# Optimization experiments

Measured on AMD Instinct MI355X. Metric: run time of the kernel, lower is better.

The kernel has to match this reference:

```python
import jax, jax.numpy as jnp
import numpy as np

B, S, C, H = 8, 1024, 768, 8
D = C // H  # head dim = 96
MLP = 4 * C


def setup_inputs() -> dict:
    key = jax.random.key(0)
    ks = jax.random.split(key, 12)
    sc = 0.02
    return {
        "x": jax.random.normal(ks[0], (B, S, C), jnp.float32),
        "ln1_w": jnp.ones((S, C), jnp.float32),
        "ln1_b": jnp.zeros((S, C), jnp.float32),
        "ln2_w": jnp.ones((S, C), jnp.float32),
        "ln2_b": jnp.zeros((S, C), jnp.float32),
        "qkv_w": jax.random.normal(ks[1], (C, 3 * C), jnp.float32) * sc,
        "proj_w": jax.random.normal(ks[2], (C, C), jnp.float32) * sc,
        "mlp_w1": jax.random.normal(ks[3], (C, MLP), jnp.float32) * sc,
        "mlp_b1": jnp.zeros((MLP,), jnp.float32),
        "mlp_w2": jax.random.normal(ks[4], (MLP, C), jnp.float32) * sc,
        "mlp_b2": jnp.zeros((C,), jnp.float32),
    }


def _layernorm2d(x, w, b, eps=1e-5):
    # normalizes over BOTH (seq, channel) dims, per nn.LayerNorm([length, channel])
    mu = jnp.mean(x, axis=(-2, -1), keepdims=True)
    var = jnp.mean(jnp.square(x - mu), axis=(-2, -1), keepdims=True)
    return (x - mu) * jax.lax.rsqrt(var + eps) * w + b


def _attention(x, qkv_w, proj_w):
    b, s, _ = x.shape
    qkv = (x @ qkv_w).reshape(b, s, 3, H, D)
    q, k, v = qkv[:, :, 0], qkv[:, :, 1], qkv[:, :, 2]  # [b, s, h, d]
    # NOTE: original module applies NO 1/sqrt(d) scaling
    scores = jnp.einsum("bshd,bthd->bhst", q, k)
    attn = jax.nn.softmax(scores, axis=-1)
    out = jnp.einsum("bhst,bthd->bshd", attn, v).reshape(b, s, C)
    return out @ proj_w


def reference(x, ln1_w, ln1_b, ln2_w, ln2_b, qkv_w, proj_w, mlp_w1, mlp_b1, mlp_w2, mlp_b2):
    # dropout is identity in eval mode
    h = x + _attention(_layernorm2d(x, ln1_w, ln1_b), qkv_w, proj_w)
    y = _layernorm2d(h, ln2_w, ln2_b)
    y = jax.nn.gelu(y @ mlp_w1 + mlp_b1, approximate=False)
    return h + (y @ mlp_w2 + mlp_b2)
```

## Files before the change

### kernel.cpp

```cpp
#include <hip/hip_runtime.h>
#include <hip/hip_bf16.h>

#define S_LEN 1024
#define NB 8
#define NC 768
#define NH 8
#define HD 96
#define NMLP 3072
#define SC (S_LEN*NC)
#define BS (NB*S_LEN)

typedef __attribute__((ext_vector_type(8))) unsigned short u16x8;
typedef __attribute__((ext_vector_type(4))) unsigned short u16x4;
typedef __attribute__((ext_vector_type(8))) __bf16 bf16x8;
typedef __attribute__((ext_vector_type(4))) float f32x4;

__device__ __forceinline__ unsigned short f2b(float f) {
  union { __hip_bfloat16 h; unsigned short u; } cvt;
  cvt.h = __float2bfloat16(f);
  return cvt.u;
}

__device__ __forceinline__ void gload16(const unsigned short* g, unsigned short* l) {
  __builtin_amdgcn_global_load_lds(
      (const __attribute__((address_space(1))) unsigned int*)g,
      (__attribute__((address_space(3))) unsigned int*)l, 16, 0, 0);
}

__device__ __forceinline__ float gelu_f(float v) {
  float u = v * (0.7978845608f + 0.0356774081f * v * v);
  float au = fabsf(u);
  float e = __expf(-2.0f * au);
  float th = (1.0f - e) / (1.0f + e);
  th = copysignf(th, u);
  return 0.5f * v * (1.0f + th);
}

template<int EPI>
__global__ __launch_bounds__(512, 1)
void gemmks(const unsigned short* __restrict__ A, int lda,
            const unsigned short* __restrict__ Bt, int ldb,
            void* __restrict__ Cv, int ldc, int K,
            const float* __restrict__ bias,
            const float* __restrict__ residual, int ldr,
            float* __restrict__ lnred)
{
  __shared__ unsigned short As[4*4096];
  __shared__ unsigned short Bs[4*8192];
  const int tid = threadIdx.x, lane = tid & 63, wid = tid >> 6;
  const int r15 = lane & 15, g = lane >> 4;
  const int tm = blockIdx.x * 128, tn = blockIdx.y * 256;
  const int NT = K >> 6;

  const int sa = lane >> 3, sc = lane & 7, slc = sc ^ sa;
  const int skc = (slc & 3) << 3;
  const int arow = wid*16 + sa*2 + ((slc >> 2) & 1);
  const unsigned short* Ag  = A  + (size_t)(tm + arow)*lda + skc;
  const unsigned short* Bg0 = Bt + (size_t)(tn + arow)*ldb + skc;
  const unsigned short* Bg1 = Bt + (size_t)(tn + 128 + arow)*ldb + skc;

  const int prl = r15 >> 1;
  const int rdo = prl*128 + (((((r15 & 1) << 2) | g) ^ prl) << 4);
  char* AsB = (char*)As; char* BsB = (char*)Bs;

#define STG(h,kk,b) { \
    gload16(Ag  + (kk) + (h)*32, As + ((b)*2+(h))*4096 + wid*512); \
    gload16(Bg0 + (kk) + (h)*32, Bs + ((b)*2+(h))*8192 + wid*512); \
    gload16(Bg1 + (kk) + (h)*32, Bs + ((b)*2+(h))*8192 + 4096 + wid*512); }
#define MFMA(a8,b8,c) __builtin_amdgcn_mfma_f32_16x16x32_bf16(a8,b8,c,0,0,0)

  f32x4 acc[8][2];
  #pragma unroll
  for (int m = 0; m < 8; ++m) {
    acc[m][0] = (f32x4){0.f,0.f,0.f,0.f};
    acc[m][1] = (f32x4){0.f,0.f,0.f,0.f};
  }

  STG(0,0,0); STG(1,0,0);

  for (int t = 0; t < NT; ++t) {
    const int rd = t & 1, wr = rd ^ 1;
    const int kk = (t + 1) << 6;
    const bool pre = (t + 1) < NT;
    #pragma unroll
    for (int h = 0; h < 2; ++h) {
      if (pre || h == 0) asm volatile("s_waitcnt vmcnt(3)" ::: "memory");
      else               asm volatile("s_waitcnt vmcnt(0)" ::: "memory");
      __builtin_amdgcn_s_barrier();
      const int ab = (rd*2 + h)*8192;
      const int bb = (rd*2 + h)*16384;
      bf16x8 a[8], b[2];
      #pragma unroll
      for (int m = 0; m < 8; ++m) a[m] = *(const bf16x8*)(AsB + ab + m*1024 + rdo);
      b[0] = *(const bf16x8*)(BsB + bb + wid*2048 + rdo);
      b[1] = *(const bf16x8*)(BsB + bb + wid*2048 + 1024 + rdo);
      if (pre) STG(h, kk, wr);
      asm volatile("s_waitcnt lgkmcnt(0)" ::: "memory");
      __builtin_amdgcn_s_setprio(1);
      #pragma unroll
      for (int m = 0; m < 8; ++m) {
        acc[m][0] = MFMA(a[m], b[0], acc[m][0]);
        acc[m][1] = MFMA(a[m], b[1], acc[m][1]);
      }
      __builtin_amdgcn_s_setprio(0);
    }
  }
#undef STG
#undef MFMA

  unsigned short* Cu = (unsigned short*)Cv;
  float* Cf = (float*)Cv;
  float s1 = 0.f, s2 = 0.f;
  #pragma unroll
  for (int m = 0; m < 8; ++m) {
    #pragma unroll
    for (int n = 0; n < 2; ++n) {
      const int col = tn + wid*32 + n*16 + r15;
      #pragma unroll
      for (int r = 0; r < 4; ++r) {
        const int row = tm + m*16 + g*4 + r;
        float v = acc[m][n][r];
        if (EPI == 2 || EPI == 4) v += bias[col];
        if (EPI == 3 || EPI == 4) v += residual[(size_t)row*ldr + col];
        if (EPI == 2) v = gelu_f(v);
        if (EPI == 3) { s1 += v; s2 += v*v; }
        if (EPI == 0 || EPI == 2) Cu[(size_t)row*ldc + col] = f2b(v);
        else                      Cf[(size_t)row*ldc + col] = v;
      }
    }
  }
  if (EPI == 3) {
    #pragma unroll
    for (int o = 32; o; o >>= 1) { s1 += __shfl_xor(s1, o); s2 += __shfl_xor(s2, o); }
    __syncthreads();
    float* red = (float*)As;
    if (lane == 0) { red[wid*2] = s1; red[wid*2+1] = s2; }
    __syncthreads();
    if (tid == 0) {
      float a1 = 0.f, a2 = 0.f;
      #pragma unroll
      for (int w = 0; w < 8; ++w) { a1 += red[w*2]; a2 += red[w*2+1]; }
      const int bidx = tm >> 10;
      atomicAdd(&lnred[bidx*2],     a1);
      atomicAdd(&lnred[bidx*2 + 1], a2);
    }
  }
}

__global__ __launch_bounds__(256, 2)
void flash_attn(const unsigned short* __restrict__ qkv,
                const unsigned short* __restrict__ vt,
                unsigned short* __restrict__ outb)
{
  __shared__ unsigned short Ks[128*96];
  __shared__ unsigned short Vs[96*128];
  __shared__ unsigned short Ps[128*128];
  const int tid = threadIdx.x, lane = tid & 63, wq = tid >> 6;
  const int r15 = lane & 15, g = lane >> 4;
  const int bh = blockIdx.y, b = bh >> 3, h = bh & 7;
  const int q0 = blockIdx.x * 128;
  const int swz = (r15 & 7) << 4;
  char* PsB = (char*)Ps;
  char* VsB = (char*)Vs;

  bf16x8 qf[2][3];
  {
    const unsigned short* qb = qkv + ((size_t)b*S_LEN + q0 + wq*32 + r15)*2304 + h*HD + g*8;
    #pragma unroll
    for (int n = 0; n < 2; ++n)
      #pragma unroll
      for (int kc = 0; kc < 3; ++kc)
        qf[n][kc] = *(const bf16x8*)(qb + (size_t)n*16*2304 + kc*32);
  }

  int krow[6], kcol[6], vrow[6], vcol[6];
  #pragma unroll
  for (int i = 0; i < 6; ++i) {
    const int c = (wq*6 + i)*64 + lane;
    krow[i] = c / 12;
    kcol[i] = (c % 12) * 8;
    const int L = c * 16;
    const int row = L >> 8, cb = L & 255;
    vrow[i] = row;
    vcol[i] = (cb ^ ((row & 7) << 4)) >> 1;
  }
  const unsigned short* kbase = qkv + (size_t)b*S_LEN*2304 + NC + h*HD;
  const unsigned short* vbase = vt + (size_t)bh*HD*S_LEN;

  f32x4 oacc[6][2];
  #pragma unroll
  for (int m = 0; m < 6; ++m) {
    oacc[m][0] = (f32x4){0.f,0.f,0.f,0.f};
    oacc[m][1] = (f32x4){0.f,0.f,0.f,0.f};
  }
  float mrun[2] = {-INFINITY, -INFINITY};
  float lrun[2] = {0.f, 0.f};

  for (int kt = 0; kt < 8; ++kt) {
    const unsigned short* ksrc = kbase + (size_t)kt*128*2304;
    const unsigned short* vsrc = vbase + kt*128;
    #pragma unroll
    for (int i = 0; i < 6; ++i) {
      gload16(ksrc + (size_t)krow[i]*2304 + kcol[i], Ks + (wq*6 + i)*512);
      gload16(vsrc + vrow[i]*1024 + vcol[i],         Vs + (wq*6 + i)*512);
    }
    __syncthreads();

    f32x4 sacc[8][2];
    #pragma unroll
    for (int m = 0; m < 8; ++m) {
      sacc[m][0] = (f32x4){0.f,0.f,0.f,0.f};
      sacc[m][1] = (f32x4){0.f,0.f,0.f,0.f};
    }
    __builtin_amdgcn_s_setprio(1);
    #pragma unroll
    for (int kc = 0; kc < 3; ++kc)
      #pragma unroll
      for (int m = 0; m < 8; ++m) {
        bf16x8 kf = *(const bf16x8*)(Ks + (m*16 + r15)*96 + kc*32 + g*8);
        sacc[m][0] = __builtin_amdgcn_mfma_f32_16x16x32_bf16(kf, qf[0][kc], sacc[m][0], 0,0,0);
        sacc[m][1] = __builtin_amdgcn_mfma_f32_16x16x32_bf16(kf, qf[1][kc], sacc[m][1], 0,0,0);
      }
    __builtin_amdgcn_s_setprio(0);

    #pragma unroll
    for (int n = 0; n < 2; ++n) {
      float pm = -INFINITY;
      #pragma unroll
      for (int m = 0; m < 8; ++m)
        #pragma unroll
        for (int r = 0; r < 4; ++r) pm = fmaxf(pm, sacc[m][n][r]);
      pm = fmaxf(pm, __shfl_xor(pm, 16));
      pm = fmaxf(pm, __shfl_xor(pm, 32));
      const float newm = fmaxf(mrun[n], pm);
      const float scale = __expf(mrun[n] - newm);
      mrun[n] = newm;
      const int qloc = wq*32 + n*16 + r15;
      float s = 0.f;
      #pragma unroll
      for (int m = 0; m < 8; ++m) {
        float e0 = __expf(sacc[m][n][0] - newm);
        float e1 = __expf(sacc[m][n][1] - newm);
        float e2 = __expf(sacc[m][n][2] - newm);
        float e3 = __expf(sacc[m][n][3] - newm);
        s += (e0 + e1) + (e2 + e3);
        u16x4 pk = { f2b(e0), f2b(e1), f2b(e2), f2b(e3) };
        *(u16x4*)(PsB + ((qloc*256 + m*32 + g*8) ^ swz)) = pk;
      }
      s += __shfl_xor(s, 16);
      s += __shfl_xor(s, 32);
      lrun[n] = lrun[n]*scale + s;
      #pragma unroll
      for (int m = 0; m < 6; ++m) oacc[m][n] *= scale;
    }

    #pragma unroll
    for (int kc = 0; kc < 4; ++kc) {
      bf16x8 pf0 = *(const bf16x8*)(PsB + (((wq*32      + r15)*256 + kc*64 + g*16) ^ swz));
      bf16x8 pf1 = *(const bf16x8*)(PsB + (((wq*32 + 16 + r15)*256 + kc*64 + g*16) ^ swz));
      __builtin_amdgcn_s_setprio(1);
      #pragma unroll
      for (int m = 0; m < 6; ++m) {
        bf16x8 vf = *(const bf16x8*)(VsB + (((m*16 + r15)*256 + kc*64 + g*16) ^ swz));
        oacc[m][0] = __builtin_amdgcn_mfma_f32_16x16x32_bf16(vf, pf0, oacc[m][0], 0,0,0);
        oacc[m][1] = __builtin_amdgcn_mfma_f32_16x16x32_bf16(vf, pf1, oacc[m][1], 0,0,0);
      }
      __builtin_amdgcn_s_setprio(0);
    }
    __syncthreads();
  }

  #pragma unroll
  for (int n = 0; n < 2; ++n) {
    const float inv = 1.0f / lrun[n];
    unsigned short* orow = outb + ((size_t)b*S_LEN + q0 + wq*32 + n*16 + r15)*NC + h*HD;
    #pragma unroll
    for (int m = 0; m < 6; ++m) {
      u16x4 pk = { f2b(oacc[m][n][0]*inv), f2b(oacc[m][n][1]*inv),
                   f2b(oacc[m][n][2]*inv), f2b(oacc[m][n][3]*inv) };
      *(u16x4*)(orow + m*16 + g*4) = pk;
    }
  }
}

__global__ void transpose_cast(const float* __restrict__ W, unsigned short* __restrict__ Wt,
                               int K, int N)
{
  __shared__ float tile[32][33];
  const int tx = threadIdx.x & 31, ty = threadIdx.x >> 5;
  const int n0 = blockIdx.x * 32, k0 = blockIdx.y * 32;
  #pragma unroll
  for (int i = 0; i < 32; i += 8)
    tile[ty + i][tx] = W[(size_t)(k0 + ty + i)*N + n0 + tx];
  __syncthreads();
  #pragma unroll
  for (int i = 0; i < 32; i += 8)
    Wt[(size_t)(n0 + ty + i)*K + k0 + tx] = f2b(tile[tx][ty + i]);
}

__global__ void transpose_v(const unsigned short* __restrict__ qkv, unsigned short* __restrict__ vt)
{
  __shared__ unsigned short tile[32][33];
  const int bh = blockIdx.z, b = bh >> 3, h = bh & 7;
  const unsigned short* v = qkv + (size_t)b*S_LEN*3*NC + 2*NC + h*HD;
  unsigned short* o = vt + (size_t)bh*HD*S_LEN;
  const int s0 = blockIdx.x * 32, d0 = blockIdx.y * 32;
  const int tx = threadIdx.x & 31, ty = threadIdx.x >> 5;
  #pragma unroll
  for (int i = 0; i < 32; i += 8)
    tile[ty + i][tx] = v[(size_t)(s0 + ty + i)*(3*NC) + d0 + tx];
  __syncthreads();
  #pragma unroll
  for (int i = 0; i < 32; i += 8)
    o[(size_t)(d0 + ty + i)*S_LEN + s0 + tx] = tile[tx][ty + i];
}

__global__ void ln_part(const float* __restrict__ X, float* __restrict__ part)
{
  const int b = blockIdx.x / 96, blk = blockIdx.x % 96;
  const float4* xb = (const float4*)(X + (size_t)b*SC);
  float s = 0.f, s2 = 0.f;
  #pragma unroll
  for (int i = 0; i < 8; ++i) {
    float4 v = xb[blk*2048 + i*256 + threadIdx.x];
    s  += v.x + v.y + v.z + v.w;
    s2 += v.x*v.x + v.y*v.y + v.z*v.z + v.w*v.w;
  }
  #pragma unroll
  for (int o = 32; o; o >>= 1) { s += __shfl_down(s, o); s2 += __shfl_down(s2, o); }
  __shared__ float r1[4], r2[4];
  const int w = threadIdx.x >> 6;
  if ((threadIdx.x & 63) == 0) { r1[w] = s; r2[w] = s2; }
  __syncthreads();
  if (threadIdx.x == 0) {
    part[(b*96 + blk)*2]     = r1[0] + r1[1] + r1[2] + r1[3];
    part[(b*96 + blk)*2 + 1] = r2[0] + r2[1] + r2[2] + r2[3];
  }
}

__global__ void ln_fin(const float* __restrict__ part, float* __restrict__ stats)
{
  const int b = blockIdx.x;
  float s = 0.f, s2 = 0.f;
  for (int i = threadIdx.x; i < 96; i += 64) {
    s  += part[(b*96 + i)*2];
    s2 += part[(b*96 + i)*2 + 1];
  }
  #pragma unroll
  for (int o = 32; o; o >>= 1) { s += __shfl_down(s, o); s2 += __shfl_down(s2, o); }
  if (threadIdx.x == 0) {
    const float inv = 1.0f / (float)SC;
    const float mu = s * inv;
    const float var = s2 * inv - mu*mu;
    stats[b*2] = mu;
    stats[b*2 + 1] = rsqrtf(var + 1e-5f);
  }
}

__global__ void ln_apply(const float* __restrict__ X, const float* __restrict__ W,
                         const float* __restrict__ Bv, const float* __restrict__ stats,
                         unsigned short* __restrict__ out)
{
  const size_t i = ((size_t)blockIdx.x*256 + threadIdx.x) * 8;
  const int b = (int)(i / SC);
  const size_t r = i % SC;
  const float mu = stats[b*2], rs = stats[b*2 + 1];
  float4 x0 = *(const float4*)(X + i),  x1 = *(const float4*)(X + i + 4);
  float4 w0 = *(const float4*)(W + r),  w1 = *(const float4*)(W + r + 4);
  float4 b0 = *(const float4*)(Bv + r), b1 = *(const float4*)(Bv + r + 4);
  u16x8 o;
  o[0] = f2b((x0.x - mu)*rs*w0.x + b0.x);
  o[1] = f2b((x0.y - mu)*rs*w0.y + b0.y);
  o[2] = f2b((x0.z - mu)*rs*w0.z + b0.z);
  o[3] = f2b((x0.w - mu)*rs*w0.w + b0.w);
  o[4] = f2b((x1.x - mu)*rs*w1.x + b1.x);
  o[5] = f2b((x1.y - mu)*rs*w1.y + b1.y);
  o[6] = f2b((x1.z - mu)*rs*w1.z + b1.z);
  o[7] = f2b((x1.w - mu)*rs*w1.w + b1.w);
  *(u16x8*)(out + i) = o;
}

__global__ void ln_apply_f(const float* __restrict__ X, const float* __restrict__ W,
                           const float* __restrict__ Bv, const float* __restrict__ red,
                           unsigned short* __restrict__ out)
{
  const size_t i = ((size_t)blockIdx.x*256 + threadIdx.x) * 8;
  const int b = (int)(i / SC);
  const size_t r = i % SC;
  const float inv = 1.0f / (float)SC;
  const float mu = red[b*2] * inv;
  const float var = red[b*2 + 1] * inv - mu*mu;
  const float rs = rsqrtf(var + 1e-5f);
  float4 x0 = *(const float4*)(X + i),  x1 = *(const float4*)(X + i + 4);
  float4 w0 = *(const float4*)(W + r),  w1 = *(const float4*)(W + r + 4);
  float4 b0 = *(const float4*)(Bv + r), b1 = *(const float4*)(Bv + r + 4);
  u16x8 o;
  o[0] = f2b((x0.x - mu)*rs*w0.x + b0.x);
  o[1] = f2b((x0.y - mu)*rs*w0.y + b0.y);
  o[2] = f2b((x0.z - mu)*rs*w0.z + b0.z);
  o[3] = f2b((x0.w - mu)*rs*w0.w + b0.w);
  o[4] = f2b((x1.x - mu)*rs*w1.x + b1.x);
  o[5] = f2b((x1.y - mu)*rs*w1.y + b1.y);
  o[6] = f2b((x1.z - mu)*rs*w1.z + b1.z);
  o[7] = f2b((x1.w - mu)*rs*w1.w + b1.w);
  *(u16x8*)(out + i) = o;
}

extern "C" void kernel_launch(void* const* d_in, const int* in_sizes, int n_in,
                              void* d_out, int out_size, void* d_ws, size_t ws_size,
                              hipStream_t stream) {
  const float* x      = (const float*)d_in[0];
  const float* ln1_w  = (const float*)d_in[1];
  const float* ln1_b  = (const float*)d_in[2];
  const float* ln2_w  = (const float*)d_in[3];
  const float* ln2_b  = (const float*)d_in[4];
  const float* qkv_w  = (const float*)d_in[5];
  const float* proj_w = (const float*)d_in[6];
  const float* mlp_w1 = (const float*)d_in[7];
  const float* mlp_b1 = (const float*)d_in[8];
  const float* mlp_w2 = (const float*)d_in[9];
  const float* mlp_b2 = (const float*)d_in[10];
  float* out = (float*)d_out;

  char* ws = (char*)d_ws;
  size_t off = 0;
  auto alloc = [&](size_t b) { size_t o = off; off += (b + 255) & ~(size_t)255; return o; };
  unsigned short* wqkvT  = (unsigned short*)(ws + alloc((size_t)3*NC*NC*2));
  unsigned short* wprojT = (unsigned short*)(ws + alloc((size_t)NC*NC*2));
  unsigned short* w1T    = (unsigned short*)(ws + alloc((size_t)NMLP*NC*2));
  unsigned short* w2T    = (unsigned short*)(ws + alloc((size_t)NC*NMLP*2));
  unsigned short* lnbf   = (unsigned short*)(ws + alloc((size_t)BS*NC*2));
  const size_t qkvOff    = alloc((size_t)BS*3*NC*2);
  unsigned short* qkvbf  = (unsigned short*)(ws + qkvOff);
  unsigned short* vt     = (unsigned short*)(ws + alloc((size_t)NB*NH*HD*S_LEN*2));
  unsigned short* ybf    = (unsigned short*)(ws + qkvOff);
  float* hbuf            = (float*)(ws + alloc((size_t)BS*NC*4));
  float* part            = (float*)(ws + alloc((size_t)NB*96*2*4));
  float* stats           = (float*)(ws + alloc((size_t)NB*2*4));
  float* lnred           = (float*)(ws + alloc((size_t)NB*2*4));
  (void)ws_size; (void)in_sizes; (void)n_in; (void)out_size;

  const dim3 blk(256);
  const dim3 blk512(512);

  hipMemsetAsync(lnred, 0, NB*2*sizeof(float), stream);

  transpose_cast<<<dim3(3*NC/32, NC/32),   blk, 0, stream>>>(qkv_w,  wqkvT,  NC, 3*NC);
  transpose_cast<<<dim3(NC/32, NC/32),     blk, 0, stream>>>(proj_w, wprojT, NC, NC);
  transpose_cast<<<dim3(NMLP/32, NC/32),   blk, 0, stream>>>(mlp_w1, w1T,    NC, NMLP);
  transpose_cast<<<dim3(NC/32, NMLP/32),   blk, 0, stream>>>(mlp_w2, w2T,    NMLP, NC);

  ln_part<<<dim3(NB*96), blk, 0, stream>>>(x, part);
  ln_fin<<<dim3(NB), dim3(64), 0, stream>>>(part, stats);
  ln_apply<<<dim3(BS*NC/2048), blk, 0, stream>>>(x, ln1_w, ln1_b, stats, lnbf);

  gemmks<0><<<dim3(BS/128, 3*NC/256), blk512, 0, stream>>>(
      lnbf, NC, wqkvT, NC, qkvbf, 3*NC, NC, nullptr, nullptr, 0, nullptr);

  transpose_v<<<dim3(S_LEN/32, HD/32, NB*NH), blk, 0, stream>>>(qkvbf, vt);

  flash_attn<<<dim3(S_LEN/128, NB*NH), blk, 0, stream>>>(qkvbf, vt, lnbf);

  gemmks<3><<<dim3(BS/128, NC/256), blk512, 0, stream>>>(
      lnbf, NC, wprojT, NC, hbuf, NC, NC, nullptr, x, NC, lnred);

  ln_apply_f<<<dim3(BS*NC/2048), blk, 0, stream>>>(hbuf, ln2_w, ln2_b, lnred, lnbf);

  gemmks<2><<<dim3(BS/128, NMLP/256), blk512, 0, stream>>>(
      lnbf, NC, w1T, NC, ybf, NMLP, NC, mlp_b1, nullptr, 0, nullptr);

  gemmks<4><<<dim3(BS/128, NC/256), blk512, 0, stream>>>(
      ybf, NMLP, w2T, NMLP, out, NC, NMLP, mlp_b2, hbuf, NC, nullptr);
}
```

Baseline: 287.3 us.

## Shrink GEMM tiles to 128x128 with 4 waves, add XCD-aware block remapping

The GEMM kernel moves from a 128x256 tile with 8 waves and one block per CU to a 128x128 tile with 4 waves and two blocks per CU. This doubles the grid and shrinks LDS per block. Block indices are remapped so consecutive tiles land on the same XCD chiplet, for both the GEMMs and flash attention, to improve L2 locality. Smaller tiles lower per-block arithmetic intensity and add more global loads of A and B, in exchange for better occupancy and wave-tail balance.

```diff
diff --git a/kernel.cpp b/kernel.cpp
--- a/kernel.cpp
+++ b/kernel.cpp
@@ -37,36 +37,43 @@
 }
 
 template<int EPI>
-__global__ __launch_bounds__(512, 1)
-void gemmks(const unsigned short* __restrict__ A, int lda,
-            const unsigned short* __restrict__ Bt, int ldb,
-            void* __restrict__ Cv, int ldc, int K,
-            const float* __restrict__ bias,
-            const float* __restrict__ residual, int ldr,
-            float* __restrict__ lnred)
+__global__ __launch_bounds__(256, 2)
+void gemmks4(const unsigned short* __restrict__ A, int lda,
+             const unsigned short* __restrict__ Bt, int ldb,
+             void* __restrict__ Cv, int ldc, int K,
+             const float* __restrict__ bias,
+             const float* __restrict__ residual, int ldr,
+             float* __restrict__ lnred)
 {
   __shared__ unsigned short As[4*4096];
-  __shared__ unsigned short Bs[4*8192];
+  __shared__ unsigned short Bs[4*4096];
   const int tid = threadIdx.x, lane = tid & 63, wid = tid >> 6;
   const int r15 = lane & 15, g = lane >> 4;
-  const int tm = blockIdx.x * 128, tn = blockIdx.y * 256;
+
+  const int nwg = gridDim.x * gridDim.y;
+  const int lin = blockIdx.y * gridDim.x + blockIdx.x;
+  const int w   = (lin & 7) * (nwg >> 3) + (lin >> 3);
+  const int tm  = (w % gridDim.x) * 128;
+  const int tn  = (w / gridDim.x) * 128;
   const int NT = K >> 6;
 
-  const int sa = lane >> 3, sc = lane & 7, slc = sc ^ sa;
+  const int sa = lane >> 3, slc = (lane & 7) ^ sa;
   const int skc = (slc & 3) << 3;
-  const int arow = wid*16 + sa*2 + ((slc >> 2) & 1);
-  const unsigned short* Ag  = A  + (size_t)(tm + arow)*lda + skc;
-  const unsigned short* Bg0 = Bt + (size_t)(tn + arow)*ldb + skc;
-  const unsigned short* Bg1 = Bt + (size_t)(tn + 128 + arow)*ldb + skc;
+  const int rwo = sa*2 + ((slc >> 2) & 1);
+  const unsigned short* Ag0 = A  + (size_t)(tm + (wid*2+0)*16 + rwo)*lda + skc;
+  const unsigned short* Ag1 = A  + (size_t)(tm + (wid*2+1)*16 + rwo)*lda + skc;
+  const unsigned short* Bg0 = Bt + (size_t)(tn + (wid*2+0)*16 + rwo)*ldb + skc;
+  const unsigned short* Bg1 = Bt + (size_t)(tn + (wid*2+1)*16 + rwo)*ldb + skc;
 
   const int prl = r15 >> 1;
   const int rdo = prl*128 + (((((r15 & 1) << 2) | g) ^ prl) << 4);
   char* AsB = (char*)As; char* BsB = (char*)Bs;
 
 #define STG(h,kk,b) { \
-    gload16(Ag  + (kk) + (h)*32, As + ((b)*2+(h))*4096 + wid*512); \
-    gload16(Bg0 + (kk) + (h)*32, Bs + ((b)*2+(h))*8192 + wid*512); \
-    gload16(Bg1 + (kk) + (h)*32, Bs + ((b)*2+(h))*8192 + 4096 + wid*512); }
+    gload16(Ag0 + (kk) + (h)*32, As + ((b)*2+(h))*4096 + (wid*2+0)*512); \
+    gload16(Ag1 + (kk) + (h)*32, As + ((b)*2+(h))*4096 + (wid*2+1)*512); \
+    gload16(Bg0 + (kk) + (h)*32, Bs + ((b)*2+(h))*4096 + (wid*2+0)*512); \
+    gload16(Bg1 + (kk) + (h)*32, Bs + ((b)*2+(h))*4096 + (wid*2+1)*512); }
 #define MFMA(a8,b8,c) __builtin_amdgcn_mfma_f32_16x16x32_bf16(a8,b8,c,0,0,0)
 
   f32x4 acc[8][2];
@@ -84,16 +91,15 @@
     const bool pre = (t + 1) < NT;
     #pragma unroll
     for (int h = 0; h < 2; ++h) {
-      if (pre || h == 0) asm volatile("s_waitcnt vmcnt(3)" ::: "memory");
+      if (pre || h == 0) asm volatile("s_waitcnt vmcnt(4)" ::: "memory");
       else               asm volatile("s_waitcnt vmcnt(0)" ::: "memory");
       __builtin_amdgcn_s_barrier();
       const int ab = (rd*2 + h)*8192;
-      const int bb = (rd*2 + h)*16384;
       bf16x8 a[8], b[2];
       #pragma unroll
       for (int m = 0; m < 8; ++m) a[m] = *(const bf16x8*)(AsB + ab + m*1024 + rdo);
-      b[0] = *(const bf16x8*)(BsB + bb + wid*2048 + rdo);
-      b[1] = *(const bf16x8*)(BsB + bb + wid*2048 + 1024 + rdo);
+      b[0] = *(const bf16x8*)(BsB + ab + wid*2048 + rdo);
+      b[1] = *(const bf16x8*)(BsB + ab + wid*2048 + 1024 + rdo);
       if (pre) STG(h, kk, wr);
       asm volatile("s_waitcnt lgkmcnt(0)" ::: "memory");
       __builtin_amdgcn_s_setprio(1);
@@ -139,7 +145,7 @@
     if (tid == 0) {
       float a1 = 0.f, a2 = 0.f;
       #pragma unroll
-      for (int w = 0; w < 8; ++w) { a1 += red[w*2]; a2 += red[w*2+1]; }
+      for (int wv = 0; wv < 4; ++wv) { a1 += red[wv*2]; a2 += red[wv*2+1]; }
       const int bidx = tm >> 10;
       atomicAdd(&lnred[bidx*2],     a1);
       atomicAdd(&lnred[bidx*2 + 1], a2);
@@ -157,8 +163,10 @@
   __shared__ unsigned short Ps[128*128];
   const int tid = threadIdx.x, lane = tid & 63, wq = tid >> 6;
   const int r15 = lane & 15, g = lane >> 4;
-  const int bh = blockIdx.y, b = bh >> 3, h = bh & 7;
-  const int q0 = blockIdx.x * 128;
+  const int lin = blockIdx.y * 8 + blockIdx.x;
+  const int w   = (lin & 7) * 64 + (lin >> 3);
+  const int bh = w >> 3, b = bh >> 3, h = bh & 7;
+  const int q0 = (w & 7) * 128;
   const int swz = (r15 & 7) << 4;
   char* PsB = (char*)Ps;
   char* VsB = (char*)Vs;
@@ -441,7 +449,6 @@
   (void)ws_size; (void)in_sizes; (void)n_in; (void)out_size;
 
   const dim3 blk(256);
-  const dim3 blk512(512);
 
   hipMemsetAsync(lnred, 0, NB*2*sizeof(float), stream);
 
@@ -454,21 +461,21 @@
   ln_fin<<<dim3(NB), dim3(64), 0, stream>>>(part, stats);
   ln_apply<<<dim3(BS*NC/2048), blk, 0, stream>>>(x, ln1_w, ln1_b, stats, lnbf);
 
-  gemmks<0><<<dim3(BS/128, 3*NC/256), blk512, 0, stream>>>(
+  gemmks4<0><<<dim3(BS/128, 3*NC/128), blk, 0, stream>>>(
       lnbf, NC, wqkvT, NC, qkvbf, 3*NC, NC, nullptr, nullptr, 0, nullptr);
 
   transpose_v<<<dim3(S_LEN/32, HD/32, NB*NH), blk, 0, stream>>>(qkvbf, vt);
 
   flash_attn<<<dim3(S_LEN/128, NB*NH), blk, 0, stream>>>(qkvbf, vt, lnbf);
 
-  gemmks<3><<<dim3(BS/128, NC/256), blk512, 0, stream>>>(
+  gemmks4<3><<<dim3(BS/128, NC/128), blk, 0, stream>>>(
       lnbf, NC, wprojT, NC, hbuf, NC, NC, nullptr, x, NC, lnred);
 
   ln_apply_f<<<dim3(BS*NC/2048), blk, 0, stream>>>(hbuf, ln2_w, ln2_b, lnred, lnbf);
 
-  gemmks<2><<<dim3(BS/128, NMLP/256), blk512, 0, stream>>>(
+  gemmks4<2><<<dim3(BS/128, NMLP/128), blk, 0, stream>>>(
       lnbf, NC, w1T, NC, ybf, NMLP, NC, mlp_b1, nullptr, 0, nullptr);
 
-  gemmks<4><<<dim3(BS/128, NC/256), blk512, 0, stream>>>(
+  gemmks4<4><<<dim3(BS/128, NMLP/128 == 0 ? 1 : NC/128), blk, 0, stream>>>(
       ybf, NMLP, w2T, NMLP, out, NC, NMLP, mlp_b2, hbuf, NC, nullptr);
 }
```

New measurement: 311.0 us. +8.3%, slower.
